# Kernel tuning notes

Hardware: AMD Instinct MI355X
Metric: run time of the kernel (lower is better)

The kernel has to match this reference:

```python
import jax, jax.numpy as jnp
import numpy as np


def setup_inputs() -> dict:
    key = jax.random.key(0)
    k1, k2, k3, k4, k5 = jax.random.split(key, 5)
    N, V, C = 4096, 4, 256
    desc = jax.random.normal(k1, (N, V, C), dtype=jnp.float32)
    sf = jax.random.normal(k2, (N, V, C), dtype=jnp.float32)
    T = jax.random.normal(k3, (V, 4, 4), dtype=jnp.float32)
    W_rec = jax.random.normal(k4, (C, C), dtype=jnp.float32) * (1.0 / np.sqrt(C))
    W_T = jax.random.normal(k5, (32, C), dtype=jnp.float32) * (1.0 / np.sqrt(32))
    return {"desc": desc, "sf": sf, "T": T, "W_rec": W_rec, "W_T": W_T}


def reference(desc, sf, T, W_rec, W_T):
    # desc, sf: [N, V, C]; T: [V, 4, 4]
    N, V, C = desc.shape
    # F.normalize(desc, dim=2)
    dn = desc / jnp.maximum(jnp.linalg.norm(desc, axis=2, keepdims=True), 1e-12)
    ar = jnp.arange(N)
    loss_total = jnp.zeros((), dtype=desc.dtype)
    count = jnp.zeros((), dtype=desc.dtype)
    for i in range(V):
        for j in range(V):
            if i == j:
                continue
            di = dn[:, i, :]  # [N, C]
            dj = dn[:, j, :]  # [N, C]
            sim = di @ dj.T   # [N, N]
            idx_ij = jnp.argmax(sim, axis=1)
            idx_ji = jnp.argmax(sim, axis=0)
            mutual = (idx_ji[idx_ij] == ar)  # [N] bool, mutual nearest neighbors
            # kpnet.reconstruction(desc_i, T_i, T_j): linear, transform-conditioned
            rel = jnp.concatenate([T[i].ravel(), T[j].ravel()])  # [32]
            sf_recon = di @ W_rec + rel @ W_T  # [N, C]
            # torch.no_grad() block -> stop_gradient
            prob = jax.nn.softmax(sim, axis=1)
            sf_j_soft = jax.lax.stop_gradient(prob @ sf[:, j, :])  # [N, C]
            m = mutual.astype(desc.dtype)[:, None]  # [N, 1]
            n_sel = jnp.sum(m)
            sq = jnp.sum(((sf_recon - sf_j_soft) ** 2) * m)
            pair_loss = sq / jnp.maximum(n_sel * C, 1.0)  # masked MSE (mean over selected elems)
            valid = (n_sel > 0).astype(desc.dtype)
            loss_total = loss_total + valid * pair_loss
            count = count + valid
    return jnp.where(count > 0, loss_total / jnp.maximum(count, 1.0), 0.0 * jnp.sum(desc))
```

## Files before the change

### kernel.cpp

```cpp
#include <hip/hip_runtime.h>
#include <math.h>

#define N_ 4096
#define V_ 4
#define C_ 256

typedef __attribute__((ext_vector_type(8))) short bf16x8;
typedef __attribute__((ext_vector_type(4))) float f32x4;
typedef unsigned long long u64;

#define OFF_R      0ull
#define OFF_DNHI   16777216ull
#define OFF_DNLO   25165824ull
#define OFF_SFT    33554432ull
#define OFF_E      37748736ull
#define OFF_ET     88080384ull
#define OFF_WTH    138412032ull
#define OFF_WTL    138543104ull
#define OFF_ROWPK  138674176ull
#define OFF_COLPK  138870784ull
#define OFF_ROWSM  139067392ull
#define OFF_COLSM  139165696ull
#define OFF_RELWT  139264000ull
#define OFF_SQ     139280384ull
#define OFF_CNT    139280448ull

__device__ __forceinline__ unsigned short f2bf(float x) {
    unsigned int u = __float_as_uint(x);
    u += 0x7fffu + ((u >> 16) & 1u);
    return (unsigned short)(u >> 16);
}
__device__ __forceinline__ float bf2f(unsigned short h) {
    return __uint_as_float(((unsigned int)h) << 16);
}
__device__ __forceinline__ f32x4 mfma16(bf16x8 a, bf16x8 b, f32x4 c) {
    return __builtin_amdgcn_mfma_f32_16x16x32_bf16(a, b, c, 0, 0, 0);
}
__device__ __forceinline__ unsigned int pk4fp8(float x0, float x1, float x2, float x3) {
    int w = 0;
    w = __builtin_amdgcn_cvt_pk_fp8_f32(x0, x1, w, false);
    w = __builtin_amdgcn_cvt_pk_fp8_f32(x2, x3, w, true);
    return (unsigned int)w;
}
__device__ __forceinline__ u64 max64(u64 a, u64 b) { return a > b ? a : b; }
__device__ __forceinline__ u64 packkey(float v, int idx) {
    return ((u64)__float_as_uint(v) << 32) | (u64)(0xFFFFFFFFu - (unsigned)idx);
}
__device__ __forceinline__ void dma16(const void* g, void* l) {
    __builtin_amdgcn_global_load_lds(
        (const __attribute__((address_space(1))) unsigned int*)g,
        (__attribute__((address_space(3))) unsigned int*)l, 16, 0, 0);
}

__global__ void normalize_k(const float* __restrict__ desc,
                            unsigned short* __restrict__ dnh, unsigned short* __restrict__ dnl) {
    int row = blockIdx.x;
    int n = row >> 2, v = row & 3;
    int c = threadIdx.x;
    float x = desc[(size_t)row * C_ + c];
    __shared__ float red[256];
    red[c] = x * x;
    __syncthreads();
    for (int s = 128; s > 0; s >>= 1) {
        if (c < s) red[c] += red[c + s];
        __syncthreads();
    }
    float inv = 1.0f / fmaxf(sqrtf(red[0]), 1e-12f);
    float y = x * inv;
    size_t o = ((size_t)v * N_ + n) * C_ + c;
    unsigned short h = f2bf(y);
    dnh[o] = h;
    dnl[o] = f2bf(y - bf2f(h));
}

__global__ void wrecT_k(const float* __restrict__ W, unsigned short* __restrict__ WTh,
                        unsigned short* __restrict__ WTl) {
    __shared__ float Tt[64 * 65];
    int k0 = blockIdx.x * 64, c0 = blockIdx.y * 64;
    int t = threadIdx.x;
    int kr = t >> 2, cq = (t & 3) * 16;
    const float* src = W + (size_t)(k0 + kr) * C_ + c0 + cq;
    for (int u = 0; u < 16; ++u) Tt[(cq + u) * 65 + kr] = src[u];
    __syncthreads();
    int cr = t >> 2, kq = (t & 3) * 16;
    unsigned short th[16] __attribute__((aligned(16)));
    unsigned short tl[16] __attribute__((aligned(16)));
    for (int u = 0; u < 16; ++u) {
        float x = Tt[cr * 65 + kq + u];
        unsigned short h = f2bf(x);
        th[u] = h; tl[u] = f2bf(x - bf2f(h));
    }
    size_t o = (size_t)(c0 + cr) * C_ + k0 + kq;
    *(uint4*)(WTh + o) = *(const uint4*)th;
    *(uint4*)(WTh + o + 8) = *(const uint4*)(th + 8);
    *(uint4*)(WTl + o) = *(const uint4*)tl;
    *(uint4*)(WTl + o + 8) = *(const uint4*)(tl + 8);
}

__global__ __launch_bounds__(256) void rmatmul_k(
    const unsigned short* __restrict__ Ah, const unsigned short* __restrict__ Al,
    const unsigned short* __restrict__ Bh, const unsigned short* __restrict__ Bl,
    float* __restrict__ R) {
    __shared__ unsigned short smem[4 * 128 * 40];
    unsigned short* sAh = smem;
    unsigned short* sAl = sAh + 128 * 40;
    unsigned short* sBh = sAl + 128 * 40;
    unsigned short* sBl = sBh + 128 * 40;
    int tid = threadIdx.x;
    int c0 = blockIdx.x * 128, m0 = blockIdx.y * 128;
    int w = tid >> 6, l = tid & 63, wm = w & 1, wn = w >> 1;
    int mr = l & 15, q = l >> 4;
    f32x4 acc[4][4];
#pragma unroll
    for (int a = 0; a < 4; ++a)
#pragma unroll
        for (int b = 0; b < 4; ++b)
#pragma unroll
            for (int u = 0; u < 4; ++u) acc[a][b][u] = 0.f;
    int r = tid >> 1, h = (tid & 1) * 16;
    for (int k0 = 0; k0 < C_; k0 += 32) {
        size_t ga = (size_t)(m0 + r) * C_ + k0 + h;
        size_t gb = (size_t)(c0 + r) * C_ + k0 + h;
        uint4 a0 = *(const uint4*)(Ah + ga);
        uint4 a1 = *(const uint4*)(Ah + ga + 8);
        uint4 a2 = *(const uint4*)(Al + ga);
        uint4 a3 = *(const uint4*)(Al + ga + 8);
        uint4 b0 = *(const uint4*)(Bh + gb);
        uint4 b1 = *(const uint4*)(Bh + gb + 8);
        uint4 b2 = *(const uint4*)(Bl + gb);
        uint4 b3 = *(const uint4*)(Bl + gb + 8);
        *(uint4*)(sAh + r * 40 + h)     = a0;
        *(uint4*)(sAh + r * 40 + h + 8) = a1;
        *(uint4*)(sAl + r * 40 + h)     = a2;
        *(uint4*)(sAl + r * 40 + h + 8) = a3;
        *(uint4*)(sBh + r * 40 + h)     = b0;
        *(uint4*)(sBh + r * 40 + h + 8) = b1;
        *(uint4*)(sBl + r * 40 + h)     = b2;
        *(uint4*)(sBl + r * 40 + h + 8) = b3;
        __syncthreads();
        bf16x8 fah[4], fal[4], fbh[4], fbl[4];
#pragma unroll
        for (int ti = 0; ti < 4; ++ti) {
            int row = wm * 64 + ti * 16 + mr;
            fah[ti] = *(const bf16x8*)(sAh + row * 40 + q * 8);
            fal[ti] = *(const bf16x8*)(sAl + row * 40 + q * 8);
        }
#pragma unroll
        for (int tj = 0; tj < 4; ++tj) {
            int row = wn * 64 + tj * 16 + mr;
            fbh[tj] = *(const bf16x8*)(sBh + row * 40 + q * 8);
            fbl[tj] = *(const bf16x8*)(sBl + row * 40 + q * 8);
        }
#pragma unroll
        for (int ti = 0; ti < 4; ++ti)
#pragma unroll
            for (int tj = 0; tj < 4; ++tj) acc[ti][tj] = mfma16(fah[ti], fbh[tj], acc[ti][tj]);
#pragma unroll
        for (int ti = 0; ti < 4; ++ti)
#pragma unroll
            for (int tj = 0; tj < 4; ++tj) acc[ti][tj] = mfma16(fah[ti], fbl[tj], acc[ti][tj]);
#pragma unroll
        for (int ti = 0; ti < 4; ++ti)
#pragma unroll
            for (int tj = 0; tj < 4; ++tj) acc[ti][tj] = mfma16(fal[ti], fbh[tj], acc[ti][tj]);
        __syncthreads();
    }
#pragma unroll
    for (int ti = 0; ti < 4; ++ti)
#pragma unroll
        for (int tj = 0; tj < 4; ++tj) {
            int c = c0 + wn * 64 + tj * 16 + mr;
#pragma unroll
            for (int rg = 0; rg < 4; ++rg) {
                int m = m0 + wm * 64 + ti * 16 + q * 4 + rg;
                R[(size_t)m * C_ + c] = acc[ti][tj][rg];
            }
        }
}

__global__ void relwt_k(const float* __restrict__ T, const float* __restrict__ WT,
                        float* __restrict__ relwt) {
    int p = blockIdx.x; int i = p >> 2, j = p & 3;
    if (i == j) return;
    int c = threadIdx.x;
    float acc = 0.f;
    for (int k = 0; k < 16; ++k) acc += T[i * 16 + k] * WT[(size_t)k * C_ + c];
    for (int k = 0; k < 16; ++k) acc += T[j * 16 + k] * WT[(size_t)(16 + k) * C_ + c];
    relwt[(size_t)p * C_ + c] = acc;
}

__global__ void sfT_k(const float* __restrict__ sf, unsigned char* __restrict__ sf8T) {
    __shared__ float Tt[64 * 65];
    int n0 = blockIdx.x * 64, c0 = blockIdx.y * 64, v = blockIdx.z;
    int t = threadIdx.x;
    int nr = t >> 2, cq = (t & 3) * 16;
    const float* src = sf + ((size_t)(n0 + nr) * V_ + v) * C_ + c0 + cq;
    for (int u = 0; u < 16; ++u) Tt[(cq + u) * 65 + nr] = src[u];
    __syncthreads();
    int cr = t >> 2, nq = (t & 3) * 16;
    unsigned int wb[4];
#pragma unroll
    for (int g = 0; g < 4; ++g) {
        const float* p = Tt + cr * 65 + nq + g * 4;
        wb[g] = pk4fp8(p[0], p[1], p[2], p[3]);
    }
    unsigned char* dst = sf8T + ((size_t)v * C_ + c0 + cr) * N_ + n0 + nq;
    *(uint4*)dst = make_uint4(wb[0], wb[1], wb[2], wb[3]);
}

__global__ void zero_k(u64* rowPk, u64* colPk, float* rowSm, float* colSm,
                       float* sq, int* cnt) {
    int idx = blockIdx.x * 256 + threadIdx.x;
    rowPk[idx] = 0ull; colPk[idx] = 0ull;
    rowSm[idx] = 0.f;  colSm[idx] = 0.f;
    if (idx < 16) { sq[idx] = 0.f; cnt[idx] = 0; }
}

__device__ __forceinline__ void dma_stage(const unsigned short* A_h, const unsigned short* A_l,
                                          const unsigned short* B_h, const unsigned short* B_l,
                                          char* lbase, int w, int laneOff, int k0) {
#pragma unroll
    for (int gg = 0; gg < 2; ++gg) {
        int g = w * 2 + gg;
        size_t go = (size_t)g * 16 * C_ + k0 + laneOff;
        char* lb = lbase + g * 1024;
        dma16(A_h + go, lb);
        dma16(A_l + go, lb + 8192);
        dma16(B_h + go, lb + 16384);
        dma16(B_l + go, lb + 24576);
    }
}

__global__ __launch_bounds__(256, 2) void sim_mfma_k(
    const unsigned short* __restrict__ dnh, const unsigned short* __restrict__ dnl,
    int ipack, int jpack, unsigned char* __restrict__ E8b, unsigned char* __restrict__ ET8b,
    u64* __restrict__ rowPkB, float* __restrict__ rowSmB,
    u64* __restrict__ colPkB, float* __restrict__ colSmB, int slotBase) {
    __shared__ char smem[65536];

    int zp = blockIdx.z;
    int iv = (ipack >> (8 * zp)) & 15;
    int jv = (jpack >> (8 * zp)) & 15;
    unsigned char* E8  = E8b  + (size_t)zp * N_ * N_;
    unsigned char* ET8 = ET8b + (size_t)zp * N_ * N_;
    int slot = slotBase + zp;
    u64*   rowPk = rowPkB + (size_t)slot * N_;
    float* rowSm = rowSmB + (size_t)slot * N_;
    u64*   colPk = colPkB + (size_t)slot * N_;
    float* colSm = colSmB + (size_t)slot * N_;

    int tid = threadIdx.x;
    int n0 = blockIdx.x * 128, m0 = blockIdx.y * 128;
    int w = tid >> 6, l = tid & 63;
    int wm = w & 1, wn = w >> 1;
    int mr = l & 15, q = l >> 4;
    int sl = q ^ ((mr >> 1) & 3);

    int rowoff = l >> 2;
    int laneOff = rowoff * C_ + (((l & 3) ^ ((rowoff >> 1) & 3)) * 8);

    const unsigned short* Ah0 = dnh + (size_t)iv * N_ * C_ + (size_t)m0 * C_;
    const unsigned short* Al0 = dnl + (size_t)iv * N_ * C_ + (size_t)m0 * C_;
    const unsigned short* Bh0 = dnh + (size_t)jv * N_ * C_ + (size_t)n0 * C_;
    const unsigned short* Bl0 = dnl + (size_t)jv * N_ * C_ + (size_t)n0 * C_;

    f32x4 acc[4][4];
#pragma unroll
    for (int a = 0; a < 4; ++a)
#pragma unroll
        for (int b = 0; b < 4; ++b)
#pragma unroll
            for (int u = 0; u < 4; ++u) acc[a][b][u] = 0.f;

    dma_stage(Ah0, Al0, Bh0, Bl0, smem, w, laneOff, 0);
    int buf = 0;
#pragma unroll 2
    for (int kc = 0; kc < 8; ++kc) {
        if (kc < 7) {
            dma_stage(Ah0, Al0, Bh0, Bl0, smem + (buf ^ 1) * 32768, w, laneOff, (kc + 1) * 32);
            asm volatile("s_waitcnt vmcnt(8)" ::: "memory");
        } else {
            asm volatile("s_waitcnt vmcnt(0)" ::: "memory");
        }
        __builtin_amdgcn_s_barrier();
        __builtin_amdgcn_sched_barrier(0);
        const unsigned short* sb = (const unsigned short*)(smem + buf * 32768);
        bf16x8 ah[4], al[4], bh[4], bl[4];
#pragma unroll
        for (int ti = 0; ti < 4; ++ti) {
            int row = wm * 64 + ti * 16 + mr;
            ah[ti] = *(const bf16x8*)(sb + row * 32 + sl * 8);
            al[ti] = *(const bf16x8*)(sb + 4096 + row * 32 + sl * 8);
        }
#pragma unroll
        for (int tj = 0; tj < 4; ++tj) {
            int row = wn * 64 + tj * 16 + mr;
            bh[tj] = *(const bf16x8*)(sb + 8192 + row * 32 + sl * 8);
            bl[tj] = *(const bf16x8*)(sb + 12288 + row * 32 + sl * 8);
        }
#pragma unroll
        for (int ti = 0; ti < 4; ++ti)
#pragma unroll
            for (int tj = 0; tj < 4; ++tj) {
                acc[ti][tj] = mfma16(ah[ti], bh[tj], acc[ti][tj]);
                acc[ti][tj] = mfma16(ah[ti], bl[tj], acc[ti][tj]);
                acc[ti][tj] = mfma16(al[ti], bh[tj], acc[ti][tj]);
            }
        __builtin_amdgcn_sched_barrier(0);
        __builtin_amdgcn_s_barrier();
        __builtin_amdgcn_sched_barrier(0);
        buf ^= 1;
    }

#pragma unroll
    for (int ti = 0; ti < 4; ++ti)
#pragma unroll
        for (int tj = 0; tj < 4; ++tj)
#pragma unroll
            for (int rg = 0; rg < 4; ++rg)
                acc[ti][tj][rg] = __expf(acc[ti][tj][rg]);

    unsigned short* S16 = (unsigned short*)smem;
#pragma unroll
    for (int ti = 0; ti < 4; ++ti)
#pragma unroll
        for (int tj = 0; tj < 4; ++tj)
#pragma unroll
            for (int rg = 0; rg < 4; ++rg)
                S16[(wm * 64 + ti * 16 + q * 4 + rg) * 132 + wn * 64 + tj * 16 + mr] =
                    f2bf(acc[ti][tj][rg]);

#pragma unroll
    for (int ti = 0; ti < 4; ++ti)
#pragma unroll
        for (int rg = 0; rg < 4; ++rg) {
            u64 best = 0ull;
#pragma unroll
            for (int tj = 0; tj < 4; ++tj)
                best = max64(best, packkey(acc[ti][tj][rg], n0 + wn * 64 + tj * 16 + mr));
            best = max64(best, __shfl_xor(best, 1));
            best = max64(best, __shfl_xor(best, 2));
            best = max64(best, __shfl_xor(best, 4));
            best = max64(best, __shfl_xor(best, 8));
            if (mr == 0) atomicMax(rowPk + m0 + wm * 64 + ti * 16 + q * 4 + rg, best);
        }
#pragma unroll
    for (int tj = 0; tj < 4; ++tj) {
        u64 best = 0ull;
#pragma unroll
        for (int ti = 0; ti < 4; ++ti)
#pragma unroll
            for (int rg = 0; rg < 4; ++rg)
                best = max64(best, packkey(acc[ti][tj][rg], m0 + wm * 64 + ti * 16 + q * 4 + rg));
        best = max64(best, __shfl_xor(best, 16));
        best = max64(best, __shfl_xor(best, 32));
        if (q == 0) atomicMax(colPk + n0 + wn * 64 + tj * 16 + mr, best);
    }
    __syncthreads();

    {
        int rr = tid & 127, hf = tid >> 7;
        const unsigned short* Sr = S16 + rr * 132 + hf * 64;
        unsigned char* dst = E8 + (size_t)(m0 + rr) * N_ + n0 + hf * 64;
        float sum = 0.f;
#pragma unroll
        for (int g = 0; g < 4; ++g) {
            unsigned int wb[4];
#pragma unroll
            for (int h2 = 0; h2 < 4; ++h2) {
                ushort4 vv = *(const ushort4*)(Sr + g * 16 + h2 * 4);
                float f0 = bf2f(vv.x), f1 = bf2f(vv.y), f2 = bf2f(vv.z), f3 = bf2f(vv.w);
                sum += (f0 + f1) + (f2 + f3);
                wb[h2] = pk4fp8(f0, f1, f2, f3);
            }
            *(uint4*)(dst + g * 16) = make_uint4(wb[0], wb[1], wb[2], wb[3]);
        }
        atomicAdd(rowSm + m0 + rr, sum);
    }
    {
        int cc = tid & 127, hf = tid >> 7;
        unsigned char* dst = ET8 + (size_t)(n0 + cc) * N_ + m0 + hf * 64;
        float sum = 0.f;
#pragma unroll
        for (int g = 0; g < 4; ++g) {
            unsigned int wb[4];
#pragma unroll
            for (int h2 = 0; h2 < 4; ++h2) {
                int rb = hf * 64 + g * 16 + h2 * 4;
                float f0 = bf2f(S16[(rb + 0) * 132 + cc]);
                float f1 = bf2f(S16[(rb + 1) * 132 + cc]);
                float f2 = bf2f(S16[(rb + 2) * 132 + cc]);
                float f3 = bf2f(S16[(rb + 3) * 132 + cc]);
                sum += (f0 + f1) + (f2 + f3);
                wb[h2] = pk4fp8(f0, f1, f2, f3);
            }
            *(uint4*)(dst + g * 16) = make_uint4(wb[0], wb[1], wb[2], wb[3]);
        }
        atomicAdd(colSm + n0 + cc, sum);
    }
}

__global__ __launch_bounds__(256) void p2_k(
    const unsigned char* __restrict__ E8b, const unsigned char* __restrict__ ET8b,
    const unsigned char* __restrict__ sf8T, int ipack, int jpack,
    const u64* __restrict__ rowPkB, const float* __restrict__ rowSmB,
    const u64* __restrict__ colPkB, const float* __restrict__ colSmB, int slotBase,
    const float* __restrict__ R, const float* __restrict__ relwt,
    float* __restrict__ pairSq, int* __restrict__ pairCnt) {
    __shared__ unsigned char sA[64 * 80];
    __shared__ unsigned char sB[128 * 80];
    __shared__ float red[256];
    __shared__ int   mutS[64];
    __shared__ float invS[64];
    int tid = threadIdx.x;
    int ct = blockIdx.x & 1, mt = blockIdx.x >> 1;
    int d = blockIdx.y & 1, zp = blockIdx.y >> 1;
    int iv = (ipack >> (8 * zp)) & 15;
    int jv = (jpack >> (8 * zp)) & 15;
    int slot = slotBase + zp;
    const unsigned char* A = (d ? ET8b : E8b) + (size_t)zp * N_ * N_;
    const unsigned char* B = sf8T + (size_t)(d ? iv : jv) * C_ * N_;
    const u64* faPk = (d ? colPkB : rowPkB) + (size_t)slot * N_;
    const u64* baPk = (d ? rowPkB : colPkB) + (size_t)slot * N_;
    const float* sumE = (d ? colSmB : rowSmB) + (size_t)slot * N_;
    const float* Rr = R + (size_t)(d ? jv : iv) * N_ * C_;
    int pid = d ? (jv * 4 + iv) : (iv * 4 + jv);
    int c0 = ct * 128, m0 = mt * 64;
    int w = tid >> 6, l = tid & 63, wm = w & 1, wn = w >> 1;
    int mr = l & 15, q = l >> 4;
    if (tid < 64) {
        int y = m0 + tid;
        unsigned faIdx = 0xFFFFFFFFu - (unsigned)(faPk[y] & 0xFFFFFFFFull);
        unsigned baIdx = 0xFFFFFFFFu - (unsigned)(baPk[faIdx] & 0xFFFFFFFFull);
        mutS[tid] = (baIdx == (unsigned)y) ? 1 : 0;
        invS[tid] = 1.0f / sumE[y];
    }
    f32x4 acc[2][4];
#pragma unroll
    for (int a = 0; a < 2; ++a)
#pragma unroll
        for (int b = 0; b < 4; ++b)
#pragma unroll
            for (int u = 0; u < 4; ++u) acc[a][b][u] = 0.f;

    int ra = tid >> 2, ka = (tid & 3) * 16;
    int rb = tid >> 1, kbb = (tid & 1) * 32;
    const unsigned char* Arow = A + (size_t)(m0 + ra) * N_ + ka;
    const unsigned char* Brow = B + (size_t)(c0 + rb) * N_ + kbb;
    uint4 pa  = *(const uint4*)(Arow);
    uint4 pb0 = *(const uint4*)(Brow);
    uint4 pb1 = *(const uint4*)(Brow + 16);
    for (int k0 = 0; k0 < N_; k0 += 64) {
        *(uint4*)(sA + ra * 80 + ka)       = pa;
        *(uint4*)(sB + rb * 80 + kbb)      = pb0;
        *(uint4*)(sB + rb * 80 + kbb + 16) = pb1;
        __syncthreads();
        int kn = k0 + 64;
        if (kn < N_) {
            pa  = *(const uint4*)(Arow + kn);
            pb0 = *(const uint4*)(Brow + kn);
            pb1 = *(const uint4*)(Brow + kn + 16);
        }
#pragma unroll
        for (int ksub = 0; ksub < 64; ksub += 32) {
            long af[2], bf[4];
#pragma unroll
            for (int ti = 0; ti < 2; ++ti)
                af[ti] = *(const long*)(sA + (wm * 32 + ti * 16 + mr) * 80 + ksub + q * 8);
#pragma unroll
            for (int tj = 0; tj < 4; ++tj)
                bf[tj] = *(const long*)(sB + (wn * 64 + tj * 16 + mr) * 80 + ksub + q * 8);
#pragma unroll
            for (int ti = 0; ti < 2; ++ti)
#pragma unroll
                for (int tj = 0; tj < 4; ++tj)
                    acc[ti][tj] = __builtin_amdgcn_mfma_f32_16x16x32_fp8_fp8(
                        af[ti], bf[tj], acc[ti][tj], 0, 0, 0);
        }
        __syncthreads();
    }
    const float* rw = relwt + (size_t)pid * C_;
    float local = 0.f;
#pragma unroll
    for (int ti = 0; ti < 2; ++ti)
#pragma unroll
        for (int tj = 0; tj < 4; ++tj) {
            int c = c0 + wn * 64 + tj * 16 + mr;
            float rwc = rw[c];
#pragma unroll
            for (int rg = 0; rg < 4; ++rg) {
                int ml = wm * 32 + ti * 16 + q * 4 + rg;
                if (mutS[ml]) {
                    int m = m0 + ml;
                    float soft = acc[ti][tj][rg] * invS[ml];
                    float dv = Rr[(size_t)m * C_ + c] + rwc - soft;
                    local += dv * dv;
                }
            }
        }
    red[tid] = local;
    __syncthreads();
    for (int s = 128; s > 0; s >>= 1) {
        if (tid < s) red[tid] += red[tid + s];
        __syncthreads();
    }
    if (tid == 0) {
        atomicAdd(pairSq + pid, red[0]);
        if (ct == 0) {
            int cnt = 0;
            for (int u = 0; u < 64; ++u) cnt += mutS[u];
            atomicAdd(pairCnt + pid, cnt);
        }
    }
}

__global__ void final_k(const float* __restrict__ sq, const int* __restrict__ cnt,
                        float* __restrict__ out) {
    if (threadIdx.x == 0 && blockIdx.x == 0) {
        float loss = 0.f, count = 0.f;
        for (int p = 0; p < 16; ++p) {
            int i = p >> 2, j = p & 3;
            if (i == j) continue;
            float ns = (float)cnt[p];
            if (ns > 0.f) { loss += sq[p] / fmaxf(ns * (float)C_, 1.0f); count += 1.f; }
        }
        out[0] = (count > 0.f) ? loss / count : 0.f;
    }
}

extern "C" void kernel_launch(void* const* d_in, const int* in_sizes, int n_in,
                              void* d_out, int out_size, void* d_ws, size_t ws_size,
                              hipStream_t stream) {
    const float* desc = (const float*)d_in[0];
    const float* sf   = (const float*)d_in[1];
    const float* T    = (const float*)d_in[2];
    const float* Wrec = (const float*)d_in[3];
    const float* WT   = (const float*)d_in[4];
    float* out = (float*)d_out;
    char* ws = (char*)d_ws;

    float*          R     = (float*)(ws + OFF_R);
    unsigned short* dnh   = (unsigned short*)(ws + OFF_DNHI);
    unsigned short* dnl   = (unsigned short*)(ws + OFF_DNLO);
    unsigned char*  sf8T  = (unsigned char*)(ws + OFF_SFT);
    unsigned char*  E8b   = (unsigned char*)(ws + OFF_E);
    unsigned char*  ET8b  = (unsigned char*)(ws + OFF_ET);
    unsigned short* WTh   = (unsigned short*)(ws + OFF_WTH);
    unsigned short* WTl   = (unsigned short*)(ws + OFF_WTL);
    u64*   rowPk = (u64*)(ws + OFF_ROWPK);
    u64*   colPk = (u64*)(ws + OFF_COLPK);
    float* rowSm = (float*)(ws + OFF_ROWSM);
    float* colSm = (float*)(ws + OFF_COLSM);
    float* relwt = (float*)(ws + OFF_RELWT);
    float* pairSq = (float*)(ws + OFF_SQ);
    int*   pairCnt = (int*)(ws + OFF_CNT);

    normalize_k<<<N_ * V_, 256, 0, stream>>>(desc, dnh, dnl);
    wrecT_k<<<dim3(4, 4), 256, 0, stream>>>(Wrec, WTh, WTl);
    rmatmul_k<<<dim3(2, 128), 256, 0, stream>>>(dnh, dnl, WTh, WTl, R);
    sfT_k<<<dim3(64, 4, 4), 256, 0, stream>>>(sf, sf8T);
    relwt_k<<<16, 256, 0, stream>>>(T, WT, relwt);
    zero_k<<<96, 256, 0, stream>>>(rowPk, colPk, rowSm, colSm, pairSq, pairCnt);

    const int ip[2] = { 0 | (0 << 8) | (0 << 16), 1 | (1 << 8) | (2 << 16) };
    const int jp[2] = { 1 | (2 << 8) | (3 << 16), 2 | (3 << 8) | (3 << 16) };
    for (int b = 0; b < 2; ++b) {
        sim_mfma_k<<<dim3(32, 32, 3), 256, 0, stream>>>(
            dnh, dnl, ip[b], jp[b], E8b, ET8b, rowPk, rowSm, colPk, colSm, b * 3);
        p2_k<<<dim3(128, 6), 256, 0, stream>>>(
            E8b, ET8b, sf8T, ip[b], jp[b], rowPk, rowSm, colPk, colSm, b * 3,
            R, relwt, pairSq, pairCnt);
    }
    final_k<<<1, 64, 0, stream>>>(pairSq, pairCnt, out);
}
```

Measured before the change: 558.3 us.

## Single-buffer sim tile LDS for higher occupancy and use f64 max for argmax keys

Drops the double-buffered LDS pipeline in the similarity GEMM and goes back to a single 32KB stage with syncthreads around each k-chunk. LDS shrinks to about 33KB and launch bounds rise to 4 blocks per CU, trading explicit load/compute overlap for more resident waves. The packed 64-bit argmax keys are also reduced with double-precision fmax instead of an integer compare. Because the exp values are positive, their bit patterns order the same way as doubles, which removes the 64-bit integer compare/select sequences.

```diff
diff --git a/kernel.cpp b/kernel.cpp
--- a/kernel.cpp
+++ b/kernel.cpp
@@ -42,9 +42,9 @@
     w = __builtin_amdgcn_cvt_pk_fp8_f32(x2, x3, w, true);
     return (unsigned int)w;
 }
-__device__ __forceinline__ u64 max64(u64 a, u64 b) { return a > b ? a : b; }
-__device__ __forceinline__ u64 packkey(float v, int idx) {
-    return ((u64)__float_as_uint(v) << 32) | (u64)(0xFFFFFFFFu - (unsigned)idx);
+__device__ __forceinline__ double packkeyd(float v, int idx) {
+    u64 k = ((u64)__float_as_uint(v) << 32) | (u64)(0xFFFFFFFFu - (unsigned)idx);
+    return __longlong_as_double((long long)k);
 }
 __device__ __forceinline__ void dma16(const void* g, void* l) {
     __builtin_amdgcn_global_load_lds(
@@ -231,12 +231,12 @@
     }
 }
 
-__global__ __launch_bounds__(256, 2) void sim_mfma_k(
+__global__ __launch_bounds__(256, 4) void sim_mfma_k(
     const unsigned short* __restrict__ dnh, const unsigned short* __restrict__ dnl,
     int ipack, int jpack, unsigned char* __restrict__ E8b, unsigned char* __restrict__ ET8b,
     u64* __restrict__ rowPkB, float* __restrict__ rowSmB,
     u64* __restrict__ colPkB, float* __restrict__ colSmB, int slotBase) {
-    __shared__ char smem[65536];
+    __shared__ char smem[33792];
 
     int zp = blockIdx.z;
     int iv = (ipack >> (8 * zp)) & 15;
@@ -272,19 +272,10 @@
 #pragma unroll
             for (int u = 0; u < 4; ++u) acc[a][b][u] = 0.f;
 
-    dma_stage(Ah0, Al0, Bh0, Bl0, smem, w, laneOff, 0);
-    int buf = 0;
-#pragma unroll 2
     for (int kc = 0; kc < 8; ++kc) {
-        if (kc < 7) {
-            dma_stage(Ah0, Al0, Bh0, Bl0, smem + (buf ^ 1) * 32768, w, laneOff, (kc + 1) * 32);
-            asm volatile("s_waitcnt vmcnt(8)" ::: "memory");
-        } else {
-            asm volatile("s_waitcnt vmcnt(0)" ::: "memory");
-        }
-        __builtin_amdgcn_s_barrier();
-        __builtin_amdgcn_sched_barrier(0);
-        const unsigned short* sb = (const unsigned short*)(smem + buf * 32768);
+        dma_stage(Ah0, Al0, Bh0, Bl0, smem, w, laneOff, kc * 32);
+        __syncthreads();
+        const unsigned short* sb = (const unsigned short*)smem;
         bf16x8 ah[4], al[4], bh[4], bl[4];
 #pragma unroll
         for (int ti = 0; ti < 4; ++ti) {
@@ -306,10 +297,7 @@
                 acc[ti][tj] = mfma16(ah[ti], bl[tj], acc[ti][tj]);
                 acc[ti][tj] = mfma16(al[ti], bh[tj], acc[ti][tj]);
             }
-        __builtin_amdgcn_sched_barrier(0);
-        __builtin_amdgcn_s_barrier();
-        __builtin_amdgcn_sched_barrier(0);
-        buf ^= 1;
+        __syncthreads();
     }
 
 #pragma unroll
@@ -334,27 +322,31 @@
     for (int ti = 0; ti < 4; ++ti)
 #pragma unroll
         for (int rg = 0; rg < 4; ++rg) {
-            u64 best = 0ull;
+            double best = 0.0;
 #pragma unroll
             for (int tj = 0; tj < 4; ++tj)
-                best = max64(best, packkey(acc[ti][tj][rg], n0 + wn * 64 + tj * 16 + mr));
-            best = max64(best, __shfl_xor(best, 1));
-            best = max64(best, __shfl_xor(best, 2));
-            best = max64(best, __shfl_xor(best, 4));
-            best = max64(best, __shfl_xor(best, 8));
-            if (mr == 0) atomicMax(rowPk + m0 + wm * 64 + ti * 16 + q * 4 + rg, best);
+                best = fmax(best, packkeyd(acc[ti][tj][rg], n0 + wn * 64 + tj * 16 + mr));
+            best = fmax(best, __shfl_xor(best, 1));
+            best = fmax(best, __shfl_xor(best, 2));
+            best = fmax(best, __shfl_xor(best, 4));
+            best = fmax(best, __shfl_xor(best, 8));
+            if (mr == 0)
+                atomicMax(rowPk + m0 + wm * 64 + ti * 16 + q * 4 + rg,
+                          (u64)__double_as_longlong(best));
         }
 #pragma unroll
     for (int tj = 0; tj < 4; ++tj) {
-        u64 best = 0ull;
+        double best = 0.0;
 #pragma unroll
         for (int ti = 0; ti < 4; ++ti)
 #pragma unroll
             for (int rg = 0; rg < 4; ++rg)
-                best = max64(best, packkey(acc[ti][tj][rg], m0 + wm * 64 + ti * 16 + q * 4 + rg));
-        best = max64(best, __shfl_xor(best, 16));
-        best = max64(best, __shfl_xor(best, 32));
-        if (q == 0) atomicMax(colPk + n0 + wn * 64 + tj * 16 + mr, best);
+                best = fmax(best, packkeyd(acc[ti][tj][rg], m0 + wm * 64 + ti * 16 + q * 4 + rg));
+        best = fmax(best, __shfl_xor(best, 16));
+        best = fmax(best, __shfl_xor(best, 32));
+        if (q == 0)
+            atomicMax(colPk + n0 + wn * 64 + tj * 16 + mr,
+                      (u64)__double_as_longlong(best));
     }
     __syncthreads();
 
```

Measured after the change: 585.7 us. +4.9%, slower.
